# Kernel optimization log

Measured on AMD Instinct MI355X. Metric: run time of the kernel, lower is better.

## Reference

```python
import jax, jax.numpy as jnp
import numpy as np

L = 16            # table_num (levels)
LOG2T = 14
T = 1 << LOG2T    # entries per table
Z = 512           # z_dim
S = 256           # style_dim
IMG = 256         # img_size
RES_MIN, RES_MAX = 16, 256
HID, OUT = 64, 3  # mlp hidden / out dims
B = 8
FDIM = 2 * L      # retrieved feature dim (2 per level)
PRIME = jnp.uint32(2654435761)  # instant-ngp hash prime
GAIN = 1.4142135623730951       # stylegan lrelu gain sqrt(2)
# geometric level resolutions res_min -> res_max
RES = np.floor(RES_MIN * np.exp(np.arange(L) * np.log(RES_MAX / RES_MIN) / (L - 1))).astype(np.float32)


def _lrelu(x):
    return GAIN * jnp.where(x >= 0, x, 0.2 * x)


def _coords():
    c = (jnp.arange(IMG, dtype=jnp.float32) + 0.5) / IMG
    x, y = jnp.meshgrid(c, c, indexing='ij')
    return jnp.stack((x, y), -1).reshape(-1, 2)  # (N, 2), N = IMG*IMG


def _mod_linear(x, s, aw, ab, w, b):
    # StyleGAN2-style modulated linear with demodulation. x: (B,N,in), s: (B,S)
    style = s @ aw + ab                                   # (B, in)
    demod = jax.lax.rsqrt((style ** 2) @ (w ** 2) + 1e-8)  # (B, out)
    return ((x * style[:, None, :]) @ w) * demod[:, None, :] + b


def _forward(z, mw0, mb0, mw1, mb1, mw2, mb2, base_tables, w_mod, b_mod,
             a0w, a0b, w0, bb0, a1w, a1b, w1, bb1, a2w, a2b, w2, bb2):
    s = _lrelu(z @ mw0 + mb0)
    s = _lrelu(s @ mw1 + mb1)
    s = _lrelu(s @ mw2 + mb2)                              # (B, S)
    # style-conditioned hash tables: per-level per-channel modulation of base tables
    scale = 1.0 + (s @ w_mod + b_mod).reshape(-1, L, 1, 2)
    tables = base_tables[None] * scale                     # (B, L, T, 2)

    coords = _coords()                                     # (N, 2)
    offs = jnp.array([[0, 0], [1, 0], [0, 1], [1, 1]], dtype=jnp.uint32)
    feats = []
    for l in range(L):
        pos = coords * RES[l]
        p0 = jnp.floor(pos)
        frac = pos - p0                                    # (N, 2)
        p0i = p0.astype(jnp.uint32)
        cx = p0i[None, :, 0] + offs[:, 0:1]                # (4, N)
        cy = p0i[None, :, 1] + offs[:, 1:2]
        idx = ((cx ^ (cy * PRIME)) & jnp.uint32(T - 1)).astype(jnp.int32)  # (4, N)
        wx = jnp.where(offs[:, 0:1] == 1, frac[None, :, 0], 1.0 - frac[None, :, 0])
        wy = jnp.where(offs[:, 1:2] == 1, frac[None, :, 1], 1.0 - frac[None, :, 1])
        wgt = wx * wy                                      # (4, N)
        tl = tables[:, l]                                  # (B, T, 2)
        f = jnp.take(tl, idx.reshape(-1), axis=1).reshape(tl.shape[0], 4, -1, 2)
        feats.append(jnp.einsum('bcnd,cn->bnd', f, wgt))   # bilinear interp
    h = jnp.concatenate(feats, -1)                         # (B, N, 2L)

    # stacked modulated MLP (3 layers), final tanh, then render to image
    h = _lrelu(_mod_linear(h, s, a0w, a0b, w0, bb0))
    h = _lrelu(_mod_linear(h, s, a1w, a1b, w1, bb1))
    h = jnp.tanh(_mod_linear(h, s, a2w, a2b, w2, bb2))     # (B, N, 3)
    return h.reshape(-1, IMG, IMG, OUT).transpose(0, 3, 1, 2)


def setup_inputs() -> dict:
    key = jax.random.key(0)
    ks = jax.random.split(key, 12)
    nrm = lambda k, sh, sc: jax.random.normal(k, sh, jnp.float32) * sc
    inp = {}
    inp['z'] = jax.random.normal(ks[0], (B, Z), jnp.float32)
    inp['mw0'] = nrm(ks[1], (Z, S), 1 / np.sqrt(Z)); inp['mb0'] = jnp.zeros((S,), jnp.float32)
    inp['mw1'] = nrm(ks[2], (S, S), 1 / np.sqrt(S)); inp['mb1'] = jnp.zeros((S,), jnp.float32)
    inp['mw2'] = nrm(ks[3], (S, S), 1 / np.sqrt(S)); inp['mb2'] = jnp.zeros((S,), jnp.float32)
    inp['base_tables'] = nrm(ks[4], (L, T, 2), 0.1)
    inp['w_mod'] = nrm(ks[5], (S, L * 2), 1 / np.sqrt(S)); inp['b_mod'] = jnp.zeros((L * 2,), jnp.float32)
    inp['a0w'] = nrm(ks[6], (S, FDIM), 1 / np.sqrt(S)); inp['a0b'] = jnp.ones((FDIM,), jnp.float32)
    inp['w0'] = nrm(ks[7], (FDIM, HID), 1 / np.sqrt(FDIM)); inp['bb0'] = jnp.zeros((HID,), jnp.float32)
    inp['a1w'] = nrm(ks[8], (S, HID), 1 / np.sqrt(S)); inp['a1b'] = jnp.ones((HID,), jnp.float32)
    inp['w1'] = nrm(ks[9], (HID, HID), 1 / np.sqrt(HID)); inp['bb1'] = jnp.zeros((HID,), jnp.float32)
    inp['a2w'] = nrm(ks[10], (S, HID), 1 / np.sqrt(S)); inp['a2b'] = jnp.ones((HID,), jnp.float32)
    inp['w2'] = nrm(ks[11], (HID, OUT), 1 / np.sqrt(HID)); inp['bb2'] = jnp.zeros((OUT,), jnp.float32)
    return inp


def reference(z, mw0, mb0, mw1, mb1, mw2, mb2, base_tables, w_mod, b_mod,
              a0w, a0b, w0, bb0, a1w, a1b, w1, bb1, a2w, a2b, w2, bb2):
    return _forward(z, mw0, mb0, mw1, mb1, mw2, mb2, base_tables, w_mod, b_mod,
                    a0w, a0b, w0, bb0, a1w, a1b, w1, bb1, a2w, a2b, w2, bb2)
```

## Files before the change

kernel.cpp:

```cpp
#include <hip/hip_runtime.h>
#include <hip/hip_bf16.h>

#define NLVL 16
#define TSZ  16384
#define NB   8

typedef _Float16 h8 __attribute__((ext_vector_type(8)));
typedef float    f4 __attribute__((ext_vector_type(4)));

#define MFMA16(A,B,C) __builtin_amdgcn_mfma_f32_16x16x32_f16(A,B,C,0,0,0)
#define GAINF 1.41421356237309515f

__device__ constexpr float RES_TAB[16] = {
  16.f, 19.f, 23.f, 27.f, 33.f, 40.f, 48.f, 58.f,
  70.f, 84.f, 101.f, 122.f, 147.f, 176.f, 212.f, 255.f
};

__device__ __forceinline__ float lrelu(float x) {
  float v = x < 0.0f ? 0.2f * x : x;
  return GAINF * v;
}
__device__ __forceinline__ float act(float x) { return fmaxf(x, 0.2f * x); }

__device__ __forceinline__ float tanh_fast(float x) {
  float t = __builtin_amdgcn_exp2f(x * 2.8853900817779268f);
  return 1.0f - 2.0f * __builtin_amdgcn_rcpf(t + 1.0f);
}

__device__ __forceinline__ unsigned pk(float a, float b) {
  union { decltype(__builtin_amdgcn_cvt_pkrtz(0.f, 0.f)) h; unsigned u; } U;
  U.h = __builtin_amdgcn_cvt_pkrtz(a, b);
  return U.u;
}

__device__ __forceinline__ void hash_features(const float* __restrict__ bt,
                                              int n, float* g)
{
  const float inv = 1.0f / 256.0f;
  float cx = ((n >> 8) + 0.5f) * inv;
  float cy = ((n & 255) + 0.5f) * inv;
#pragma unroll
  for (int l = 0; l < NLVL; ++l) {
    float res = RES_TAB[l];
    float px = cx * res, py = cy * res;
    float fx0 = floorf(px), fy0 = floorf(py);
    float fx = px - fx0, fy = py - fy0;
    unsigned x0 = (unsigned)fx0, y0 = (unsigned)fy0;
    unsigned hy0 = y0 * 2654435761u;
    unsigned hy1 = (y0 + 1u) * 2654435761u;
    unsigned i00 = (x0 ^ hy0) & 16383u;
    unsigned i10 = ((x0 + 1u) ^ hy0) & 16383u;
    unsigned i01 = (x0 ^ hy1) & 16383u;
    unsigned i11 = ((x0 + 1u) ^ hy1) & 16383u;
    const float2* tb = (const float2*)(bt + (size_t)l * (TSZ * 2));
    float2 f00 = tb[i00], f10 = tb[i10], f01 = tb[i01], f11 = tb[i11];
    float wx0 = 1.0f - fx, wy0 = 1.0f - fy;
    float w00 = wx0 * wy0, w10 = fx * wy0, w01 = wx0 * fy, w11 = fx * fy;
    g[2 * l]     = w00 * f00.x + w10 * f10.x + w01 * f01.x + w11 * f11.x;
    g[2 * l + 1] = w00 * f00.y + w10 * f10.y + w01 * f01.y + w11 * f11.y;
  }
}

__device__ __forceinline__ void map_layer(const float* __restrict__ xs_in,
                                          float* __restrict__ out_lds,
                                          const float* __restrict__ W,
                                          const float* __restrict__ bias,
                                          int K, int t,
                                          float* __restrict__ part)
{
  const int j4 = (t & 63) * 4;
  const int ks = t >> 6;
  const int chunk = K >> 2;
  const int kb = ks * chunk;
  f4 a0 = {0,0,0,0}, a1 = {0,0,0,0}, a2 = {0,0,0,0}, a3 = {0,0,0,0};
#pragma unroll 4
  for (int k = 0; k < chunk; k += 4) {
    f4 w0 = *(const f4*)&W[(kb + k + 0) * 256 + j4];
    f4 w1 = *(const f4*)&W[(kb + k + 1) * 256 + j4];
    f4 w2 = *(const f4*)&W[(kb + k + 2) * 256 + j4];
    f4 w3 = *(const f4*)&W[(kb + k + 3) * 256 + j4];
    float x0 = xs_in[kb + k + 0], x1 = xs_in[kb + k + 1];
    float x2 = xs_in[kb + k + 2], x3 = xs_in[kb + k + 3];
    a0 += x0 * w0; a1 += x1 * w1; a2 += x2 * w2; a3 += x3 * w3;
  }
  *(f4*)&part[ks * 256 + j4] = (a0 + a1) + (a2 + a3);
  __syncthreads();
  {
    float v = part[t] + part[256 + t] + part[512 + t] + part[768 + t];
    out_lds[t] = lrelu(bias[t] + v);
  }
  __syncthreads();
}

__global__ void __launch_bounds__(256) k_pre(
    const float* __restrict__ z,
    const float* __restrict__ mw0, const float* __restrict__ mb0,
    const float* __restrict__ mw1, const float* __restrict__ mb1,
    const float* __restrict__ mw2, const float* __restrict__ mb2,
    const float* __restrict__ bt,
    const float* __restrict__ w_mod, const float* __restrict__ b_mod,
    const float* __restrict__ a0w, const float* __restrict__ a0b,
    const float* __restrict__ w0,
    const float* __restrict__ a1w, const float* __restrict__ a1b,
    const float* __restrict__ w1,
    const float* __restrict__ a2w, const float* __restrict__ a2b,
    const float* __restrict__ w2,
    _Float16* __restrict__ W0h, _Float16* __restrict__ W1h,
    _Float16* __restrict__ W2h, _Float16* __restrict__ ghf)
{
  __shared__ float xs[512];
  __shared__ float sA[256], sB[256];
  __shared__ float part[1024];
  __shared__ float st0[32], scf[32], st1[64], st2[64];
  __shared__ float dm0[64], dm1[64], dm2[3];

  const int t = threadIdx.x;

  if (blockIdx.x >= 8) {
    int n = (blockIdx.x - 8) * 256 + t;
    float gl[32];
    hash_features(bt, n, gl);
    int tile = n >> 4, c = n & 15;
#pragma unroll
    for (int gg = 0; gg < 4; ++gg) {
      union { unsigned u[4]; uint4 v; } U;
      U.u[0] = pk(gl[8 * gg + 0], gl[8 * gg + 1]);
      U.u[1] = pk(gl[8 * gg + 2], gl[8 * gg + 3]);
      U.u[2] = pk(gl[8 * gg + 4], gl[8 * gg + 5]);
      U.u[3] = pk(gl[8 * gg + 6], gl[8 * gg + 7]);
      *(uint4*)&ghf[(size_t)tile * 512 + (gg * 16 + c) * 8] = U.v;
    }
    return;
  }

  const int b = blockIdx.x;

  for (int k = t; k < 512; k += 256) xs[k] = z[b * 512 + k];
  __syncthreads();

  map_layer(xs, sA, mw0, mb0, 512, t, part);
  map_layer(sA, sB, mw1, mb1, 256, t, part);
  map_layer(sB, xs, mw2, mb2, 256, t, part);
  const float* ss = xs;

  if (t < 32) {
    float as = a0b[t], am = b_mod[t];
    for (int k = 0; k < 256; ++k) {
      float sv = ss[k];
      as = fmaf(sv, a0w[k * 32 + t], as);
      am = fmaf(sv, w_mod[k * 32 + t], am);
    }
    st0[t] = as; scf[t] = 1.0f + am;
  }
  if (t >= 64 && t < 128) {
    int j = t - 64; float v = a1b[j];
    for (int k = 0; k < 256; ++k) v = fmaf(ss[k], a1w[k * 64 + j], v);
    st1[j] = v;
  }
  if (t >= 128 && t < 192) {
    int j = t - 128; float v = a2b[j];
    for (int k = 0; k < 256; ++k) v = fmaf(ss[k], a2w[k * 64 + j], v);
    st2[j] = v;
  }
  __syncthreads();
  if (t < 64) {
    float acc = 1e-8f;
    for (int i = 0; i < 32; ++i) { float p = st0[i] * w0[i * 64 + t]; acc = fmaf(p, p, acc); }
    dm0[t] = 1.0f / sqrtf(acc);
  }
  if (t >= 64 && t < 128) {
    int j = t - 64; float acc = 1e-8f;
    for (int k = 0; k < 64; ++k) { float p = st1[k] * w1[k * 64 + j]; acc = fmaf(p, p, acc); }
    dm1[j] = 1.0f / sqrtf(acc);
  }
  if (t >= 192 && t < 195) {
    int ch = t - 192; float acc = 1e-8f;
    for (int k = 0; k < 64; ++k) { float p = st2[k] * w2[k * 3 + ch]; acc = fmaf(p, p, acc); }
    dm2[ch] = 1.0f / sqrtf(acc);
  }
  __syncthreads();

  for (int f = t; f < 2048; f += 256) {
    int j = f >> 5, i = f & 31;
    W0h[b * 2048 + f] = (_Float16)(scf[i] * st0[i] * w0[i * 64 + j] * dm0[j]);
  }
  for (int f = t; f < 4096; f += 256) {
    int j2 = f >> 6, k = f & 63;
    W1h[b * 4096 + f] = (_Float16)(GAINF * st1[k] * w1[k * 64 + j2] * dm1[j2]);
  }
  for (int f = t; f < 1024; f += 256) {
    int ch = f >> 6, k = f & 63;
    W2h[b * 1024 + f] = (ch < 3) ? (_Float16)(GAINF * st2[k] * w2[k * 3 + ch] * dm2[ch])
                                 : (_Float16)0.0f;
  }
}

__device__ __forceinline__ void st4(_Float16* L, int pix, int jb, f4 v) {
  int ks = jb ^ ((pix & 7) << 3);
  union { unsigned u[2]; uint2 v2; } U;
  U.u[0] = pk(v[0], v[1]); U.u[1] = pk(v[2], v[3]);
  *(uint2*)(L + pix * 64 + ks) = U.v2;
}
__device__ __forceinline__ h8 ldf(const _Float16* L, int pix, int kb) {
  int ks = kb ^ ((pix & 7) << 3);
  return *(const h8*)(L + pix * 64 + ks);
}

template <int FUSED>
__global__ void __launch_bounds__(256) k_mlp(
    const _Float16* __restrict__ W0h, const _Float16* __restrict__ W1h,
    const _Float16* __restrict__ W2h, const _Float16* __restrict__ ghf,
    const float* __restrict__ bt,
    const float* __restrict__ bb0, const float* __restrict__ bb1,
    const float* __restrict__ bb2, float* __restrict__ out)
{
  __shared__ _Float16 lds[4][4096];
  __shared__ _Float16 hb[FUSED ? 8192 : 8];

  const int t = threadIdx.x;
  const int w = t >> 6, lane = t & 63;
  const int c = lane & 15, g = lane >> 4;
  const int b = blockIdx.y;
  const int pixb = blockIdx.x * 256 + w * 64;
  const int tile0 = pixb >> 4;
  _Float16* L = lds[w];

  if constexpr (FUSED) {
    float gl[32];
    hash_features(bt, blockIdx.x * 256 + t, gl);
    int tl = t >> 4, cl = t & 15;
#pragma unroll
    for (int gg = 0; gg < 4; ++gg) {
      union { unsigned u[4]; uint4 v; } U;
      U.u[0] = pk(gl[8 * gg + 0], gl[8 * gg + 1]);
      U.u[1] = pk(gl[8 * gg + 2], gl[8 * gg + 3]);
      U.u[2] = pk(gl[8 * gg + 4], gl[8 * gg + 5]);
      U.u[3] = pk(gl[8 * gg + 6], gl[8 * gg + 7]);
      *(uint4*)&hb[tl * 512 + (gg * 16 + cl) * 8] = U.v;
    }
    __syncthreads();
  }

  h8 A0[4], A1[4][2], A2[2];
#pragma unroll
  for (int jt = 0; jt < 4; ++jt)
    A0[jt] = *(const h8*)&W0h[b * 2048 + (jt * 16 + c) * 32 + 8 * g];
#pragma unroll
  for (int jt = 0; jt < 4; ++jt)
#pragma unroll
    for (int kf = 0; kf < 2; ++kf)
      A1[jt][kf] = *(const h8*)&W1h[b * 4096 + (jt * 16 + c) * 64 + kf * 32 + 8 * g];
#pragma unroll
  for (int kf = 0; kf < 2; ++kf)
    A2[kf] = *(const h8*)&W2h[b * 1024 + c * 64 + kf * 32 + 8 * g];

  f4 bv0[4], bv1[4], bv2;
#pragma unroll
  for (int jt = 0; jt < 4; ++jt) {
    bv0[jt] = *(const f4*)&bb0[jt * 16 + 4 * g];
    bv1[jt] = *(const f4*)&bb1[jt * 16 + 4 * g];
  }
  if (g == 0) { bv2 = f4{bb2[0], bb2[1], bb2[2], 0.0f}; }
  else        { bv2 = f4{0.0f, 0.0f, 0.0f, 0.0f}; }

  f4 acc[4][4];
#pragma unroll
  for (int pt = 0; pt < 4; ++pt) {
    h8 Bh;
    if constexpr (FUSED) {
      Bh = *(const h8*)&hb[(w * 4 + pt) * 512 + lane * 8];
    } else {
      Bh = *(const h8*)&ghf[(size_t)(tile0 + pt) * 512 + lane * 8];
    }
#pragma unroll
    for (int jt = 0; jt < 4; ++jt)
      acc[jt][pt] = MFMA16(A0[jt], Bh, bv0[jt]);
  }

#pragma unroll
  for (int jt = 0; jt < 4; ++jt)
#pragma unroll
    for (int pt = 0; pt < 4; ++pt) {
      f4 v = acc[jt][pt];
#pragma unroll
      for (int r = 0; r < 4; ++r) v[r] = act(v[r]);
      st4(L, pt * 16 + c, jt * 16 + 4 * g, v);
    }

  f4 acc1[4][4];
#pragma unroll
  for (int pt = 0; pt < 4; ++pt) {
    h8 Bf0 = ldf(L, pt * 16 + c, 0 * 32 + 8 * g);
    h8 Bf1 = ldf(L, pt * 16 + c, 1 * 32 + 8 * g);
#pragma unroll
    for (int jt = 0; jt < 4; ++jt) {
      f4 a = MFMA16(A1[jt][0], Bf0, bv1[jt]);
      acc1[jt][pt] = MFMA16(A1[jt][1], Bf1, a);
    }
  }

#pragma unroll
  for (int jt = 0; jt < 4; ++jt)
#pragma unroll
    for (int pt = 0; pt < 4; ++pt) {
      f4 v = acc1[jt][pt];
#pragma unroll
      for (int r = 0; r < 4; ++r) v[r] = act(v[r]);
      st4(L, pt * 16 + c, jt * 16 + 4 * g, v);
    }

#pragma unroll
  for (int pt = 0; pt < 4; ++pt) {
    h8 Bf0 = ldf(L, pt * 16 + c, 0 * 32 + 8 * g);
    h8 Bf1 = ldf(L, pt * 16 + c, 1 * 32 + 8 * g);
    f4 a = MFMA16(A2[0], Bf0, bv2);
    a = MFMA16(A2[1], Bf1, a);
    if (g == 0) {
      int pix = pixb + pt * 16 + c;
#pragma unroll
      for (int r = 0; r < 3; ++r)
        out[((b * 3 + r) << 16) + pix] = tanh_fast(a[r]);
    }
  }
}

extern "C" void kernel_launch(void* const* d_in, const int* in_sizes, int n_in,
                              void* d_out, int out_size, void* d_ws, size_t ws_size,
                              hipStream_t stream)
{
  const float* z    = (const float*)d_in[0];
  const float* mw0  = (const float*)d_in[1];
  const float* mb0  = (const float*)d_in[2];
  const float* mw1  = (const float*)d_in[3];
  const float* mb1  = (const float*)d_in[4];
  const float* mw2  = (const float*)d_in[5];
  const float* mb2  = (const float*)d_in[6];
  const float* bt   = (const float*)d_in[7];
  const float* wmod = (const float*)d_in[8];
  const float* bmod = (const float*)d_in[9];
  const float* a0w  = (const float*)d_in[10];
  const float* a0b  = (const float*)d_in[11];
  const float* w0   = (const float*)d_in[12];
  const float* bb0  = (const float*)d_in[13];
  const float* a1w  = (const float*)d_in[14];
  const float* a1b  = (const float*)d_in[15];
  const float* w1   = (const float*)d_in[16];
  const float* bb1  = (const float*)d_in[17];
  const float* a2w  = (const float*)d_in[18];
  const float* a2b  = (const float*)d_in[19];
  const float* w2   = (const float*)d_in[20];
  const float* bb2  = (const float*)d_in[21];

  char* ws = (char*)d_ws;
  _Float16* W0h = (_Float16*)(ws);
  _Float16* W1h = (_Float16*)(ws + 32768);
  _Float16* W2h = (_Float16*)(ws + 98304);
  _Float16* ghf = (_Float16*)(ws + 114688);
  float* out = (float*)d_out;

  k_pre<<<8 + 256, 256, 0, stream>>>(z, mw0, mb0, mw1, mb1, mw2, mb2, bt,
                                     wmod, bmod, a0w, a0b, w0,
                                     a1w, a1b, w1, a2w, a2b, w2,
                                     W0h, W1h, W2h, ghf);

  if (ws_size >= (size_t)4308992) {
    k_mlp<0><<<dim3(256, NB), 256, 0, stream>>>(W0h, W1h, W2h, ghf, bt,
                                                bb0, bb1, bb2, out);
  } else {
    k_mlp<1><<<dim3(256, NB), 256, 0, stream>>>(W0h, W1h, W2h, ghf, bt,
                                                bb0, bb1, bb2, out);
  }
}
```

Baseline: 46.32 us.

## Warm L2 with weights from hash blocks and split style projections across threads

The hash-feature blocks now each stream a slice of the mapping and style weight matrices into cache with dummy XOR loads, so the 8 per-batch blocks that run the serial mapping MLP hit in L2 instead of DRAM. The style/affine projections, which used to run as 256-iteration loops on 32-64 threads, are now split across all 256 threads with a k-partition and a shared-memory reduction. This adds extra global traffic and an extra barrier, and relies on the prefetching blocks running before the mapping blocks read those weights.

After: 45.32 us. -2.2%, faster.

```diff
diff --git a/kernel.cpp b/kernel.cpp
--- a/kernel.cpp
+++ b/kernel.cpp
@@ -61,6 +61,17 @@
   }
 }
 
+__device__ __forceinline__ void pf_slice(const float* __restrict__ p, int nf4,
+                                         int s, int t, uint2& sink)
+{
+  int per = nf4 >> 5;
+  const uint4* q = (const uint4*)p + (size_t)s * per;
+  for (int e = t; e < per; e += 256) {
+    uint4 v = q[e];
+    sink.x ^= v.x; sink.y ^= v.w;
+  }
+}
+
 __device__ __forceinline__ void map_layer(const float* __restrict__ xs_in,
                                           float* __restrict__ out_lds,
                                           const float* __restrict__ W,
@@ -117,6 +128,25 @@
   const int t = threadIdx.x;
 
   if (blockIdx.x >= 8) {
+    int s = (blockIdx.x - 8) >> 3;
+    uint2 sink = {0, 0};
+    pf_slice(mw0,  32768, s, t, sink);
+    pf_slice(mw1,  16384, s, t, sink);
+    pf_slice(mw2,  16384, s, t, sink);
+    pf_slice(w_mod, 2048, s, t, sink);
+    pf_slice(a0w,   2048, s, t, sink);
+    pf_slice(a1w,   4096, s, t, sink);
+    pf_slice(a2w,   4096, s, t, sink);
+    pf_slice(w0,     512, s, t, sink);
+    pf_slice(w1,    1024, s, t, sink);
+    if (s == 0) {
+      const uint4* q = (const uint4*)w2;
+      for (int e = t; e < 48; e += 256) { uint4 v = q[e]; sink.x ^= v.x; }
+      const uint4* qb = (const uint4*)mb0;
+      for (int e = t; e < 64; e += 256) { uint4 v = qb[e]; sink.y ^= v.y; }
+    }
+    asm volatile("" :: "v"(sink.x), "v"(sink.y));
+
     int n = (blockIdx.x - 8) * 256 + t;
     float gl[32];
     hash_features(bt, n, gl);
@@ -143,26 +173,44 @@
   map_layer(sB, xs, mw2, mb2, 256, t, part);
   const float* ss = xs;
 
+  {
+    const int j = t & 31, kb = (t >> 5) * 32;
+    float am = 0.f, as = 0.f;
+#pragma unroll 8
+    for (int k = 0; k < 32; ++k) {
+      float sv = ss[kb + k];
+      am = fmaf(sv, w_mod[(kb + k) * 32 + j], am);
+      as = fmaf(sv, a0w[(kb + k) * 32 + j], as);
+    }
+    part[t] = am; part[256 + t] = as;
+  }
+  {
+    const int j = t & 63, kb = (t >> 6) * 64;
+    float v1 = 0.f, v2 = 0.f;
+#pragma unroll 8
+    for (int k = 0; k < 64; ++k) {
+      float sv = ss[kb + k];
+      v1 = fmaf(sv, a1w[(kb + k) * 64 + j], v1);
+      v2 = fmaf(sv, a2w[(kb + k) * 64 + j], v2);
+    }
+    part[512 + t] = v1; part[768 + t] = v2;
+  }
+  __syncthreads();
   if (t < 32) {
-    float as = a0b[t], am = b_mod[t];
-    for (int k = 0; k < 256; ++k) {
-      float sv = ss[k];
-      as = fmaf(sv, a0w[k * 32 + t], as);
-      am = fmaf(sv, w_mod[k * 32 + t], am);
-    }
-    st0[t] = as; scf[t] = 1.0f + am;
-  }
-  if (t >= 64 && t < 128) {
-    int j = t - 64; float v = a1b[j];
-    for (int k = 0; k < 256; ++k) v = fmaf(ss[k], a1w[k * 64 + j], v);
-    st1[j] = v;
+    float am = b_mod[t], as = a0b[t];
+#pragma unroll
+    for (int q = 0; q < 8; ++q) { am += part[q * 32 + t]; as += part[256 + q * 32 + t]; }
+    scf[t] = 1.0f + am; st0[t] = as;
   }
   if (t >= 128 && t < 192) {
-    int j = t - 128; float v = a2b[j];
-    for (int k = 0; k < 256; ++k) v = fmaf(ss[k], a2w[k * 64 + j], v);
-    st2[j] = v;
-  }
-  __syncthreads();
+    int j = t - 128;
+    float v1 = a1b[j], v2 = a2b[j];
+#pragma unroll
+    for (int q = 0; q < 4; ++q) { v1 += part[512 + q * 64 + j]; v2 += part[768 + q * 64 + j]; }
+    st1[j] = v1; st2[j] = v2;
+  }
+  __syncthreads();
+
   if (t < 64) {
     float acc = 1e-8f;
     for (int i = 0; i < 32; ++i) { float p = st0[i] * w0[i * 64 + t]; acc = fmaf(p, p, acc); }
```
